# Optimization experiments

Measured on AMD Instinct MI355X. Metric: run time of the kernel, lower is better.

The kernel has to match this reference:

```python
import jax, jax.numpy as jnp
import numpy as np

DIM = 1024
HEADS = 8
DIM_HEAD = 64
INNER = HEADS * DIM_HEAD
SCALE = DIM_HEAD ** -0.5


def setup_inputs() -> dict:
    key = jax.random.key(0)
    ks = jax.random.split(key, 6)
    b, n = 2, 2048
    x = jax.random.normal(ks[0], (b, n, DIM), dtype=jnp.float32)
    rel_pos_bias = jax.random.normal(ks[1], (HEADS, n, n), dtype=jnp.float32)
    # learned params (Linear stores W as [out, in]; we keep [in, out] for x @ W)
    Wq = jax.random.normal(ks[2], (DIM, INNER), dtype=jnp.float32) * (DIM ** -0.5)
    Wkv = jax.random.normal(ks[3], (DIM, 2 * DIM_HEAD), dtype=jnp.float32) * (DIM ** -0.5)
    Wo = jax.random.normal(ks[4], (INNER, DIM), dtype=jnp.float32) * (INNER ** -0.5)
    bo = jax.random.normal(ks[5], (DIM,), dtype=jnp.float32) * 0.01
    return {"x": x, "rel_pos_bias": rel_pos_bias, "Wq": Wq, "Wkv": Wkv, "Wo": Wo, "bo": bo}


def reference(x, rel_pos_bias, Wq, Wkv, Wo, bo):
    b, n, _ = x.shape
    q = x @ Wq                       # [b, n, h*d]
    kv = x @ Wkv                     # [b, n, 2d] (multi-query: single shared kv head)
    k, v = kv[..., :DIM_HEAD], kv[..., DIM_HEAD:]
    q = q.reshape(b, n, HEADS, DIM_HEAD).transpose(0, 2, 1, 3) * SCALE  # [b, h, n, d]
    sim = jnp.einsum('bhid,bjd->bhij', q, k)
    sim = sim + rel_pos_bias         # bias broadcast over batch
    causal_mask = jnp.triu(jnp.ones((n, n), dtype=bool), k=1)
    neg = -jnp.finfo(sim.dtype).max
    sim = jnp.where(causal_mask, neg, sim)
    attn = jax.nn.softmax(sim, axis=-1)  # stable softmax (max-subtract internally)
    out = jnp.einsum('bhij,bjd->bhid', attn, v)
    out = out.transpose(0, 2, 1, 3).reshape(b, n, INNER)  # [b, n, h*d]
    return out @ Wo + bo
```

## Files before the change

kernel.cpp:

```cpp
#include <hip/hip_runtime.h>

#define NSEQ 2048
#define NB 2
#define NH 8
#define HD 64
#define DMODEL 1024
#define DINNER 512

#define SLOT_F 4224

typedef __attribute__((ext_vector_type(8))) short bf16x8;
typedef __attribute__((ext_vector_type(4))) float f32x4;

__device__ __forceinline__ ushort f2bf(float f) {
  uint u = __float_as_uint(f);
  uint r = (u + 0x7fffu + ((u >> 16) & 1u)) >> 16;
  return (ushort)r;
}

__device__ __forceinline__ void gld16(const ushort* g, ushort* l) {
  __builtin_amdgcn_global_load_lds(
      (const __attribute__((address_space(1))) uint*)g,
      (__attribute__((address_space(3))) uint*)l, 16, 0, 0);
}

__global__ __launch_bounds__(256) void transpose_cast_both_kernel(
    const float* __restrict__ Wq, const float* __restrict__ Wkv,
    const float* __restrict__ Wo, ushort* __restrict__ WT1sw,
    ushort* __restrict__ WoTsw) {
  __shared__ float t[64][65];
  const int id = blockIdx.x;
  const float *srcA, *srcB;
  int ldA, ldB, nsplit, k0, n0;
  ushort* tile;
  if (id < 160) {
    const int nt = id >> 4, kt = id & 15;
    k0 = kt * 64; n0 = nt * 64;
    srcA = Wq; srcB = Wkv; ldA = 512; ldB = 128; nsplit = 512;
    tile = WT1sw + (size_t)(nt * 16 + kt) * 4096;
  } else {
    const int u = id - 160;
    const int nt = u >> 3, kt = u & 7;
    k0 = kt * 64; n0 = nt * 64;
    srcA = Wo; srcB = Wo; ldA = 1024; ldB = 1024; nsplit = 1024;
    tile = WoTsw + (size_t)(nt * 8 + kt) * 4096;
  }
  const float* src; int ld, nb;
  if (n0 < nsplit) { src = srcA; ld = ldA; nb = n0; }
  else { src = srcB; ld = ldB; nb = n0 - nsplit; }
  const int r = threadIdx.x >> 4;
  const int c = (threadIdx.x & 15) * 4;
#pragma unroll
  for (int rr = r; rr < 64; rr += 16) {
    float4 v = *(const float4*)(src + (size_t)(k0 + rr) * ld + nb + c);
    t[rr][c + 0] = v.x; t[rr][c + 1] = v.y; t[rr][c + 2] = v.z; t[rr][c + 3] = v.w;
  }
  __syncthreads();
#pragma unroll
  for (int rr = r; rr < 64; rr += 16) {
    ushort4 o;
    o.x = f2bf(t[c + 0][rr]); o.y = f2bf(t[c + 1][rr]);
    o.z = f2bf(t[c + 2][rr]); o.w = f2bf(t[c + 3][rr]);
    *(ushort4*)(tile + (size_t)rr * 64 + (((c >> 3) ^ (rr & 7)) << 3) + (c & 7)) = o;
  }
}

__device__ __forceinline__ void stageA_f32(const float* __restrict__ src, int ld,
                                           int row0, int k0, ushort* lds, int tid) {
#pragma unroll
  for (int i = 0; i < 4; ++i) {
    const int cix = i * 256 + tid;
    const int row = cix >> 3, j = cix & 7;
    const float* p = src + (size_t)(row0 + row) * ld + k0 + j * 8;
    float4 a = *(const float4*)p;
    float4 b = *(const float4*)(p + 4);
    uint u0, u1, u2, u3;
    asm("v_cvt_pk_bf16_f32 %0, %1, %2" : "=v"(u0) : "v"(a.x), "v"(a.y));
    asm("v_cvt_pk_bf16_f32 %0, %1, %2" : "=v"(u1) : "v"(a.z), "v"(a.w));
    asm("v_cvt_pk_bf16_f32 %0, %1, %2" : "=v"(u2) : "v"(b.x), "v"(b.y));
    asm("v_cvt_pk_bf16_f32 %0, %1, %2" : "=v"(u3) : "v"(b.z), "v"(b.w));
    uint4 v; v.x = u0; v.y = u1; v.z = u2; v.w = u3;
    *(uint4*)((char*)lds + row * 128 + ((j ^ (row & 7)) << 4)) = v;
  }
}

__global__ __launch_bounds__(256) void qkv_mfma_kernel(
    const float* __restrict__ x, const ushort* __restrict__ WT1sw,
    ushort* __restrict__ qb, ushort* __restrict__ ksw, ushort* __restrict__ vsw) {
  __shared__ ushort As[128 * 64];
  __shared__ ushort Bs[64 * 64];
  const int tid = threadIdx.x;
  const int m0 = blockIdx.x * 128;
  const int nt = blockIdx.y;
  const int lane = tid & 63;
  const int w = tid >> 6;
  const int wr = w >> 1, wc = w & 1;
  const int lr = lane & 15, lg = lane >> 4;
  f32x4 acc[4][2];
#pragma unroll
  for (int a = 0; a < 4; ++a)
#pragma unroll
    for (int b = 0; b < 2; ++b) acc[a][b] = (f32x4){0.f, 0.f, 0.f, 0.f};
  for (int kt = 0; kt < 16; ++kt) {
    __syncthreads();
    {
      const ushort* bsrc =
          WT1sw + (size_t)(nt * 16 + kt) * 4096 + w * 1024 + lane * 8;
      gld16(bsrc, Bs + w * 1024);
      gld16(bsrc + 512, Bs + w * 1024 + 512);
    }
    stageA_f32(x, DMODEL, m0, kt * 64, As, tid);
    __syncthreads();
#pragma unroll
    for (int kk = 0; kk < 2; ++kk) {
      bf16x8 af[4], bfr[2];
#pragma unroll
      for (int mi = 0; mi < 4; ++mi) {
        const int r = wr * 64 + mi * 16 + lr;
        af[mi] = *(const bf16x8*)((char*)As + r * 128 + (((kk * 4 + lg) ^ (r & 7)) << 4));
      }
#pragma unroll
      for (int ni = 0; ni < 2; ++ni) {
        const int r = wc * 32 + ni * 16 + lr;
        bfr[ni] = *(const bf16x8*)((char*)Bs + r * 128 + (((kk * 4 + lg) ^ (r & 7)) << 4));
      }
#pragma unroll
      for (int mi = 0; mi < 4; ++mi)
#pragma unroll
        for (int ni = 0; ni < 2; ++ni)
          acc[mi][ni] = __builtin_amdgcn_mfma_f32_16x16x32_bf16(af[mi], bfr[ni],
                                                                acc[mi][ni], 0, 0, 0);
    }
  }
#pragma unroll
  for (int mi = 0; mi < 4; ++mi)
#pragma unroll
    for (int ni = 0; ni < 2; ++ni) {
      const int n = nt * 64 + wc * 32 + ni * 16 + lr;
#pragma unroll
      for (int r = 0; r < 4; ++r) {
        const int m = m0 + wr * 64 + mi * 16 + lg * 4 + r;
        const int bb = m >> 11, key = m & (NSEQ - 1);
        const float v = acc[mi][ni][r];
        if (nt < 8) {
          const int h = n >> 6, d = n & 63;
          qb[((size_t)((bb * NH + h) * NSEQ) + key) * HD + d] = f2bf(v * 0.125f);
        } else if (nt == 8) {
          const int d = n - DINNER;
          const int t = key >> 6, row = key & 63;
          ksw[(size_t)((bb * 32 + t) * 64 + row) * 64 +
              (((d >> 3) ^ (row & 7)) << 3) + (d & 7)] = f2bf(v);
        } else {
          const int d = n - DINNER - HD;
          const int pr = key >> 7, kk = key & 127;
          vsw[(size_t)((bb * 16 + pr) * 64 + d) * 128 +
              (((kk >> 3) ^ (d & 15)) << 3) + (kk & 7)] = f2bf(v);
        }
      }
    }
}

__global__ __launch_bounds__(256) void out_mfma_kernel(
    const ushort* __restrict__ obsw, const ushort* __restrict__ WoTsw,
    const float* __restrict__ bo, float* __restrict__ out) {
  __shared__ ushort As[2 * 128 * 64];
  __shared__ ushort Bs[2 * 64 * 64];
  const int tid = threadIdx.x;
  const int mt = blockIdx.x;
  const int nt = blockIdx.y;
  const int lane = tid & 63;
  const int w = tid >> 6;
  const int wr = w >> 1, wc = w & 1;
  const int lr = lane & 15, lg = lane >> 4;
  f32x4 acc[4][2];
#pragma unroll
  for (int a = 0; a < 4; ++a)
#pragma unroll
    for (int b = 0; b < 2; ++b) acc[a][b] = (f32x4){0.f, 0.f, 0.f, 0.f};

#define OISSUE(kt, buf)                                                       \
  {                                                                           \
    const ushort* _as =                                                       \
        obsw + (size_t)(mt * 8 + (kt)) * 8192 + w * 2048 + lane * 8;          \
    ushort* _ad = As + (buf) * 8192 + w * 2048;                               \
    gld16(_as, _ad);                                                          \
    gld16(_as + 512, _ad + 512);                                              \
    gld16(_as + 1024, _ad + 1024);                                            \
    gld16(_as + 1536, _ad + 1536);                                            \
    const ushort* _bs =                                                       \
        WoTsw + (size_t)(nt * 8 + (kt)) * 4096 + w * 1024 + lane * 8;         \
    ushort* _bd = Bs + (buf) * 4096 + w * 1024;                               \
    gld16(_bs, _bd);                                                          \
    gld16(_bs + 512, _bd + 512);                                              \
  }

  OISSUE(0, 0);
  OISSUE(1, 1);
  int cur = 0;
  for (int i = 0; i < 8; ++i) {
    if (i < 7) {
      asm volatile("s_waitcnt vmcnt(6)" ::: "memory");
    } else {
      asm volatile("s_waitcnt vmcnt(0)" ::: "memory");
    }
    __builtin_amdgcn_sched_barrier(0);
    __builtin_amdgcn_s_barrier();
    const char* Ac = (const char*)(As + cur * 8192);
    const char* Bc = (const char*)(Bs + cur * 4096);
    __builtin_amdgcn_s_setprio(1);
#pragma unroll
    for (int kk = 0; kk < 2; ++kk) {
      bf16x8 af[4], bfr[2];
#pragma unroll
      for (int mi = 0; mi < 4; ++mi) {
        const int r = wr * 64 + mi * 16 + lr;
        af[mi] = *(const bf16x8*)(Ac + r * 128 + (((kk * 4 + lg) ^ (r & 7)) << 4));
      }
#pragma unroll
      for (int ni = 0; ni < 2; ++ni) {
        const int r = wc * 32 + ni * 16 + lr;
        bfr[ni] = *(const bf16x8*)(Bc + r * 128 + (((kk * 4 + lg) ^ (r & 7)) << 4));
      }
#pragma unroll
      for (int mi = 0; mi < 4; ++mi)
#pragma unroll
        for (int ni = 0; ni < 2; ++ni)
          acc[mi][ni] = __builtin_amdgcn_mfma_f32_16x16x32_bf16(af[mi], bfr[ni],
                                                                acc[mi][ni], 0, 0, 0);
    }
    __builtin_amdgcn_s_setprio(0);
    __builtin_amdgcn_sched_barrier(0);
    __builtin_amdgcn_s_barrier();
    if (i + 2 < 8) OISSUE(i + 2, cur);
    cur ^= 1;
  }
#undef OISSUE
#pragma unroll
  for (int mi = 0; mi < 4; ++mi)
#pragma unroll
    for (int ni = 0; ni < 2; ++ni) {
      const int n = nt * 64 + wc * 32 + ni * 16 + lr;
      const float bias = bo[n];
#pragma unroll
      for (int r = 0; r < 4; ++r) {
        const int m = mt * 128 + wr * 64 + mi * 16 + lg * 4 + r;
        out[(size_t)m * DMODEL + n] = acc[mi][ni][r] + bias;
      }
    }
}

__global__ __launch_bounds__(256) void attn_mfma_kernel(
    const ushort* __restrict__ qb, const ushort* __restrict__ ksw,
    const ushort* __restrict__ vsw, const float* __restrict__ rpb,
    ushort* __restrict__ obsw, float* __restrict__ scratch) {
  __shared__ ushort Ks[2 * 128 * 64];
  __shared__ ushort Vs[2 * 64 * 128];
  __shared__ ushort Ps[4 * 16 * 128];
  const int tid = threadIdx.x;
  const int lane = tid & 63;
  const int w = tid >> 6;
  const int id = blockIdx.x;
  const int bh = id & 15;
  int qt, ch, p0, p1, partial;
  if (id < 256) {
    qt = 16 + (id >> 4); ch = 0; p0 = 0; p1 = 8; partial = 1;
  } else if (id < 512) {
    qt = 31 - ((id - 256) >> 4); ch = 1; p0 = 8; p1 = (qt >> 1) + 1; partial = 1;
  } else {
    qt = 15 - ((id - 512) >> 4); ch = 0; p0 = 0; p1 = (qt >> 1) + 1; partial = 0;
  }
  const int bb = bh >> 3, h = bh & 7;
  const int q0 = qt * 64;
  const int lr = lane & 15;
  const int lg = lane >> 4;
  const int pdiag = qt >> 1;

  const ushort* kpair = ksw + (size_t)bb * 32 * 64 * 64;
  const ushort* vpair = vsw + (size_t)bb * 16 * 64 * 128;
  const ushort* ksrcw = kpair + w * 2048 + lane * 8;
  const ushort* vsrcw = vpair + w * 2048 + lane * 8;
  ushort* kdstw = Ks + w * 2048;
  ushort* vdstw = Vs + w * 2048;

#define ISSUE(pp, bsel)                                                     \
  {                                                                         \
    const ushort* _ks = ksrcw + (size_t)(pp) * 8192;                        \
    const ushort* _vs = vsrcw + (size_t)(pp) * 8192;                        \
    ushort* _kd = kdstw + (bsel) * 8192;                                    \
    ushort* _vd = vdstw + (bsel) * 8192;                                    \
    gld16(_ks + 0 * 512, _kd + 0 * 512);                                    \
    gld16(_ks + 1 * 512, _kd + 1 * 512);                                    \
    gld16(_ks + 2 * 512, _kd + 2 * 512);                                    \
    gld16(_ks + 3 * 512, _kd + 3 * 512);                                    \
    gld16(_vs + 0 * 512, _vd + 0 * 512);                                    \
    gld16(_vs + 1 * 512, _vd + 1 * 512);                                    \
    gld16(_vs + 2 * 512, _vd + 2 * 512);                                    \
    gld16(_vs + 3 * 512, _vd + 3 * 512);                                    \
  }

#define LOAD_BIAS(pp, dst)                                                  \
  {                                                                         \
    const float* _br = rpb + (size_t)h * NSEQ * NSEQ +                      \
                       (size_t)(q0 + w * 16 + lg * 4) * NSEQ +              \
                       (pp) * 128 + lr;                                     \
    _Pragma("unroll")                                                       \
    for (int _ct = 0; _ct < 8; ++_ct)                                       \
      _Pragma("unroll")                                                     \
      for (int _r = 0; _r < 4; ++_r)                                        \
        dst[_ct][_r] = _br[(size_t)_r * NSEQ + _ct * 16];                   \
  }

  bf16x8 qf[2];
  {
    const ushort* qrow =
        qb + ((size_t)(bh * NSEQ) + q0 + w * 16 + lr) * HD + lg * 8;
    qf[0] = *(const bf16x8*)qrow;
    qf[1] = *(const bf16x8*)(qrow + 32);
  }
  f32x4 oacc[4];
  float m_run[4], l_run[4];
#pragma unroll
  for (int r = 0; r < 4; ++r) { m_run[r] = -1e30f; l_run[r] = 0.f; }
#pragma unroll
  for (int dt = 0; dt < 4; ++dt) oacc[dt] = (f32x4){0.f, 0.f, 0.f, 0.f};

  float bias_c[8][4], bias_n[8][4];

  ISSUE(p0, 0);
  LOAD_BIAS(p0, bias_c);
  ISSUE(p0 + 1, 1);
  int curb = 0;

  for (int p = p0; p < p1; ++p) {
    if (p < p1 - 1) {
      asm volatile("s_waitcnt vmcnt(40)" ::: "memory");
    } else {
      asm volatile("s_waitcnt vmcnt(32)" ::: "memory");
    }
    __builtin_amdgcn_sched_barrier(0);
    __builtin_amdgcn_s_barrier();

    const char* Kc = (const char*)(Ks + curb * 8192);
    const char* Vc = (const char*)(Vs + curb * 8192);
    f32x4 s[8];
    __builtin_amdgcn_s_setprio(1);
#pragma unroll
    for (int ct = 0; ct < 8; ++ct) {
      s[ct] = (f32x4){0.f, 0.f, 0.f, 0.f};
      const int krow = ct * 16 + lr;
#pragma unroll
      for (int kk = 0; kk < 2; ++kk) {
        bf16x8 kf = *(const bf16x8*)(Kc + krow * 128 +
                                     (((kk * 4 + lg) ^ (krow & 7)) << 4));
        s[ct] = __builtin_amdgcn_mfma_f32_16x16x32_bf16(qf[kk], kf, s[ct], 0, 0, 0);
      }
    }
    __builtin_amdgcn_s_setprio(0);
    if (p + 1 < p1) LOAD_BIAS(p + 1, bias_n);
#pragma unroll
    for (int ct = 0; ct < 8; ++ct)
#pragma unroll
      for (int r = 0; r < 4; ++r) s[ct][r] += bias_c[ct][r];
    if (p == pdiag) {
      const int qrel = q0 + w * 16 + lg * 4;
#pragma unroll
      for (int ct = 0; ct < 8; ++ct) {
        const int kg = p * 128 + ct * 16 + lr;
#pragma unroll
        for (int r = 0; r < 4; ++r)
          if (kg > qrel + r) s[ct][r] = -1e30f;
      }
    }
    float fac[4];
#pragma unroll
    for (int r = 0; r < 4; ++r) {
      float mt = s[0][r];
#pragma unroll
      for (int ct = 1; ct < 8; ++ct) mt = fmaxf(mt, s[ct][r]);
#pragma unroll
      for (int msk = 1; msk < 16; msk <<= 1)
        mt = fmaxf(mt, __shfl_xor(mt, msk, 64));
      const float m_new = fmaxf(m_run[r], mt);
      fac[r] = __expf(m_run[r] - m_new);
      m_run[r] = m_new;
      float ls = 0.f;
#pragma unroll
      for (int ct = 0; ct < 8; ++ct) {
        const float pv = __expf(s[ct][r] - m_new);
        s[ct][r] = pv;
        ls += pv;
      }
#pragma unroll
      for (int msk = 1; msk < 16; msk <<= 1) ls += __shfl_xor(ls, msk, 64);
      l_run[r] = l_run[r] * fac[r] + ls;
    }
#pragma unroll
    for (int dt = 0; dt < 4; ++dt)
#pragma unroll
      for (int r = 0; r < 4; ++r) oacc[dt][r] *= fac[r];
    char* Pw = (char*)Ps + w * 4096;
#pragma unroll
    for (int ct = 0; ct < 8; ++ct) {
      uint u01, u23;
      asm("v_cvt_pk_bf16_f32 %0, %1, %2" : "=v"(u01) : "v"(s[ct][0]), "v"(s[ct][1]));
      asm("v_cvt_pk_bf16_f32 %0, %1, %2" : "=v"(u23) : "v"(s[ct][2]), "v"(s[ct][3]));
      const int cbyte = (ct * 16 + lr) * 2;
      const int chv = cbyte >> 4, off = cbyte & 15;
      const int r0 = lg * 4;
      *(ushort*)(Pw + (r0 + 0) * 256 + (((chv ^ (r0 + 0)) << 4) | off)) = (ushort)u01;
      *(ushort*)(Pw + (r0 + 1) * 256 + (((chv ^ (r0 + 1)) << 4) | off)) = (ushort)(u01 >> 16);
      *(ushort*)(Pw + (r0 + 2) * 256 + (((chv ^ (r0 + 2)) << 4) | off)) = (ushort)u23;
      *(ushort*)(Pw + (r0 + 3) * 256 + (((chv ^ (r0 + 3)) << 4) | off)) = (ushort)(u23 >> 16);
    }
    __builtin_amdgcn_s_setprio(1);
#pragma unroll
    for (int kk = 0; kk < 4; ++kk) {
      bf16x8 pf = *(const bf16x8*)(Pw + lr * 256 + (((kk * 4 + lg) ^ lr) << 4));
#pragma unroll
      for (int dt = 0; dt < 4; ++dt) {
        const int vrow = dt * 16 + lr;
        bf16x8 vf = *(const bf16x8*)(Vc + vrow * 256 +
                                     (((kk * 4 + lg) ^ (vrow & 15)) << 4));
        oacc[dt] =
            __builtin_amdgcn_mfma_f32_16x16x32_bf16(pf, vf, oacc[dt], 0, 0, 0);
      }
    }
    __builtin_amdgcn_s_setprio(0);
    __builtin_amdgcn_sched_barrier(0);
    __builtin_amdgcn_s_barrier();
    if (p + 2 < p1) ISSUE(p + 2, curb);
    if (p + 1 < p1) {
#pragma unroll
      for (int ct = 0; ct < 8; ++ct)
#pragma unroll
        for (int r = 0; r < 4; ++r) bias_c[ct][r] = bias_n[ct][r];
    }
    curb ^= 1;
  }
#undef ISSUE
#undef LOAD_BIAS
  if (!partial) {
#pragma unroll
    for (int r = 0; r < 4; ++r) {
      const int qg = q0 + w * 16 + lg * 4 + r;
      const int m = bb * NSEQ + qg;
      const int row = m & 127, mt = m >> 7;
      const int rs = row & 7;
      ushort* tb = obsw + (size_t)(mt * 8 + h) * 8192 + row * 64;
      const float inv = 1.0f / l_run[r];
#pragma unroll
      for (int dt = 0; dt < 4; ++dt) {
        const int d = dt * 16 + lr;
        tb[(((d >> 3) ^ rs) << 3) + (d & 7)] = f2bf(oacc[dt][r] * inv);
      }
    }
  } else {
    float* slot =
        scratch + (size_t)((bh * 16 + (qt - 16)) * 2 + ch) * SLOT_F;
#pragma unroll
    for (int r = 0; r < 4; ++r) {
      const int row = w * 16 + lg * 4 + r;
#pragma unroll
      for (int dt = 0; dt < 4; ++dt)
        slot[row * 64 + dt * 16 + lr] = oacc[dt][r];
      if (lr == 0) {
        slot[4096 + row] = m_run[r];
        slot[4160 + row] = l_run[r];
      }
    }
  }
}

__global__ __launch_bounds__(256) void attn_merge_kernel(
    const float* __restrict__ scratch, ushort* __restrict__ obsw) {
  const int bid = blockIdx.x;
  const int bh = bid >> 4;
  const int qt = 16 + (bid & 15);
  const int bb = bh >> 3, h = bh & 7;
  const float* s0 = scratch + (size_t)((bh * 16 + (qt - 16)) * 2) * SLOT_F;
  const float* s1 = s0 + SLOT_F;
  const int t = threadIdx.x;
  const int r = t >> 2;
  const int c0 = (t & 3) * 16;
  const float m0 = s0[4096 + r], m1 = s1[4096 + r];
  const float M = fmaxf(m0, m1);
  const float sc0 = __expf(m0 - M), sc1 = __expf(m1 - M);
  const float L = s0[4160 + r] * sc0 + s1[4160 + r] * sc1;
  const float inv = 1.0f / L;
  ushort tmp[16];
#pragma unroll
  for (int j4 = 0; j4 < 4; ++j4) {
    float4 a = *(const float4*)(s0 + r * 64 + c0 + j4 * 4);
    float4 b = *(const float4*)(s1 + r * 64 + c0 + j4 * 4);
    tmp[j4 * 4 + 0] = f2bf((a.x * sc0 + b.x * sc1) * inv);
    tmp[j4 * 4 + 1] = f2bf((a.y * sc0 + b.y * sc1) * inv);
    tmp[j4 * 4 + 2] = f2bf((a.z * sc0 + b.z * sc1) * inv);
    tmp[j4 * 4 + 3] = f2bf((a.w * sc0 + b.w * sc1) * inv);
  }
  const int m = bb * NSEQ + qt * 64 + r;
  const int row = m & 127, mt = m >> 7;
  const int rs = row & 7;
  ushort* tb = obsw + (size_t)(mt * 8 + h) * 8192 + row * 64;
  *(uint4*)(tb + ((((c0 >> 3) + 0) ^ rs) << 3)) = *(const uint4*)&tmp[0];
  *(uint4*)(tb + ((((c0 >> 3) + 1) ^ rs) << 3)) = *(const uint4*)&tmp[8];
}

extern "C" void kernel_launch(void* const* d_in, const int* in_sizes, int n_in,
                              void* d_out, int out_size, void* d_ws, size_t ws_size,
                              hipStream_t stream) {
  (void)in_sizes; (void)n_in; (void)out_size; (void)ws_size;
  const float* x = (const float*)d_in[0];
  const float* rpb = (const float*)d_in[1];
  const float* Wq = (const float*)d_in[2];
  const float* Wkv = (const float*)d_in[3];
  const float* Wo = (const float*)d_in[4];
  const float* bo = (const float*)d_in[5];
  float* out = (float*)d_out;

  ushort* qbb = (ushort*)d_ws;
  ushort* ksw = qbb + (size_t)NB * NH * NSEQ * HD;
  ushort* vsw = ksw + (size_t)NB * NSEQ * HD;
  ushort* obsw = vsw + (size_t)NB * NSEQ * HD;
  ushort* WT1sw = obsw + (size_t)NB * NSEQ * DINNER;
  ushort* WoTsw = WT1sw + (size_t)640 * DMODEL;
  float* scratch = (float*)(WoTsw + (size_t)DMODEL * DINNER);

  transpose_cast_both_kernel<<<dim3(288), 256, 0, stream>>>(Wq, Wkv, Wo, WT1sw,
                                                            WoTsw);
  qkv_mfma_kernel<<<dim3(32, 10), 256, 0, stream>>>(x, WT1sw, qbb, ksw, vsw);
  attn_mfma_kernel<<<dim3(768), 256, 0, stream>>>(qbb, ksw, vsw, rpb, obsw,
                                                  scratch);
  attn_merge_kernel<<<dim3(256), 256, 0, stream>>>(scratch, obsw);
  out_mfma_kernel<<<dim3(32, 16), 256, 0, stream>>>(obsw, WoTsw, bo, out);
}
```

Measured before the change: 83.04 us.

## Pre-cast x to swizzled bf16 and widen QKV/out GEMM tiles to 128x128

x is now converted to bf16 once, in swizzled tiles inside the prep kernel, so the QKV GEMM no longer re-reads and converts fp32 x for every N tile. The QKV GEMM now uses double-buffered async global-to-LDS loads with a software pipeline like the out GEMM. Both GEMMs move from 128x64 to 128x128 block tiles, halving their grid sizes and raising reuse of each loaded tile. In exchange there is an extra bf16 round trip of x through memory, more accumulator registers, more LDS per block, and fewer blocks, which can lower occupancy.

```diff
diff --git a/kernel.cpp b/kernel.cpp
--- a/kernel.cpp
+++ b/kernel.cpp
@@ -24,22 +24,45 @@
       (__attribute__((address_space(3))) uint*)l, 16, 0, 0);
 }
 
-__global__ __launch_bounds__(256) void transpose_cast_both_kernel(
-    const float* __restrict__ Wq, const float* __restrict__ Wkv,
-    const float* __restrict__ Wo, ushort* __restrict__ WT1sw,
+__global__ __launch_bounds__(256) void prep_kernel(
+    const float* __restrict__ x, const float* __restrict__ Wq,
+    const float* __restrict__ Wkv, const float* __restrict__ Wo,
+    ushort* __restrict__ xsw, ushort* __restrict__ WT1sw,
     ushort* __restrict__ WoTsw) {
   __shared__ float t[64][65];
   const int id = blockIdx.x;
+  const int tid = threadIdx.x;
+  if (id < 512) {
+    const int mt = id >> 4, kt = id & 15;
+    ushort* tile = xsw + (size_t)(mt * 16 + kt) * 8192;
+#pragma unroll
+    for (int i = 0; i < 4; ++i) {
+      const int cix = i * 256 + tid;
+      const int row = cix >> 3, j = cix & 7;
+      const float* p = x + (size_t)(mt * 128 + row) * DMODEL + kt * 64 + j * 8;
+      float4 a = *(const float4*)p;
+      float4 b = *(const float4*)(p + 4);
+      uint u0, u1, u2, u3;
+      asm("v_cvt_pk_bf16_f32 %0, %1, %2" : "=v"(u0) : "v"(a.x), "v"(a.y));
+      asm("v_cvt_pk_bf16_f32 %0, %1, %2" : "=v"(u1) : "v"(a.z), "v"(a.w));
+      asm("v_cvt_pk_bf16_f32 %0, %1, %2" : "=v"(u2) : "v"(b.x), "v"(b.y));
+      asm("v_cvt_pk_bf16_f32 %0, %1, %2" : "=v"(u3) : "v"(b.z), "v"(b.w));
+      uint4 v; v.x = u0; v.y = u1; v.z = u2; v.w = u3;
+      *(uint4*)(tile + (size_t)row * 64 + ((j ^ (row & 7)) << 3)) = v;
+    }
+    return;
+  }
   const float *srcA, *srcB;
   int ldA, ldB, nsplit, k0, n0;
   ushort* tile;
-  if (id < 160) {
-    const int nt = id >> 4, kt = id & 15;
+  if (id < 672) {
+    const int u = id - 512;
+    const int nt = u >> 4, kt = u & 15;
     k0 = kt * 64; n0 = nt * 64;
     srcA = Wq; srcB = Wkv; ldA = 512; ldB = 128; nsplit = 512;
     tile = WT1sw + (size_t)(nt * 16 + kt) * 4096;
   } else {
-    const int u = id - 160;
+    const int u = id - 672;
     const int nt = u >> 3, kt = u & 7;
     k0 = kt * 64; n0 = nt * 64;
     srcA = Wo; srcB = Wo; ldA = 1024; ldB = 1024; nsplit = 1024;
@@ -48,8 +71,8 @@
   const float* src; int ld, nb;
   if (n0 < nsplit) { src = srcA; ld = ldA; nb = n0; }
   else { src = srcB; ld = ldB; nb = n0 - nsplit; }
-  const int r = threadIdx.x >> 4;
-  const int c = (threadIdx.x & 15) * 4;
+  const int r = tid >> 4;
+  const int c = (tid & 15) * 4;
 #pragma unroll
   for (int rr = r; rr < 64; rr += 16) {
     float4 v = *(const float4*)(src + (size_t)(k0 + rr) * ld + nb + c);
@@ -65,87 +88,98 @@
   }
 }
 
-__device__ __forceinline__ void stageA_f32(const float* __restrict__ src, int ld,
-                                           int row0, int k0, ushort* lds, int tid) {
-#pragma unroll
-  for (int i = 0; i < 4; ++i) {
-    const int cix = i * 256 + tid;
-    const int row = cix >> 3, j = cix & 7;
-    const float* p = src + (size_t)(row0 + row) * ld + k0 + j * 8;
-    float4 a = *(const float4*)p;
-    float4 b = *(const float4*)(p + 4);
-    uint u0, u1, u2, u3;
-    asm("v_cvt_pk_bf16_f32 %0, %1, %2" : "=v"(u0) : "v"(a.x), "v"(a.y));
-    asm("v_cvt_pk_bf16_f32 %0, %1, %2" : "=v"(u1) : "v"(a.z), "v"(a.w));
-    asm("v_cvt_pk_bf16_f32 %0, %1, %2" : "=v"(u2) : "v"(b.x), "v"(b.y));
-    asm("v_cvt_pk_bf16_f32 %0, %1, %2" : "=v"(u3) : "v"(b.z), "v"(b.w));
-    uint4 v; v.x = u0; v.y = u1; v.z = u2; v.w = u3;
-    *(uint4*)((char*)lds + row * 128 + ((j ^ (row & 7)) << 4)) = v;
-  }
-}
-
 __global__ __launch_bounds__(256) void qkv_mfma_kernel(
-    const float* __restrict__ x, const ushort* __restrict__ WT1sw,
+    const ushort* __restrict__ xsw, const ushort* __restrict__ WT1sw,
     ushort* __restrict__ qb, ushort* __restrict__ ksw, ushort* __restrict__ vsw) {
-  __shared__ ushort As[128 * 64];
-  __shared__ ushort Bs[64 * 64];
+  __shared__ ushort As[2 * 128 * 64];
+  __shared__ ushort Bs[2 * 128 * 64];
   const int tid = threadIdx.x;
-  const int m0 = blockIdx.x * 128;
+  const int mt = blockIdx.x;
   const int nt = blockIdx.y;
   const int lane = tid & 63;
   const int w = tid >> 6;
   const int wr = w >> 1, wc = w & 1;
   const int lr = lane & 15, lg = lane >> 4;
-  f32x4 acc[4][2];
+  f32x4 acc[4][4];
 #pragma unroll
   for (int a = 0; a < 4; ++a)
 #pragma unroll
-    for (int b = 0; b < 2; ++b) acc[a][b] = (f32x4){0.f, 0.f, 0.f, 0.f};
-  for (int kt = 0; kt < 16; ++kt) {
-    __syncthreads();
-    {
-      const ushort* bsrc =
-          WT1sw + (size_t)(nt * 16 + kt) * 4096 + w * 1024 + lane * 8;
-      gld16(bsrc, Bs + w * 1024);
-      gld16(bsrc + 512, Bs + w * 1024 + 512);
-    }
-    stageA_f32(x, DMODEL, m0, kt * 64, As, tid);
-    __syncthreads();
+    for (int b = 0; b < 4; ++b) acc[a][b] = (f32x4){0.f, 0.f, 0.f, 0.f};
+
+#define QISSUE(kt, buf)                                                       \
+  {                                                                           \
+    const ushort* _as =                                                       \
+        xsw + (size_t)(mt * 16 + (kt)) * 8192 + w * 2048 + lane * 8;          \
+    ushort* _ad = As + (buf) * 8192 + w * 2048;                               \
+    gld16(_as, _ad);                                                          \
+    gld16(_as + 512, _ad + 512);                                              \
+    gld16(_as + 1024, _ad + 1024);                                            \
+    gld16(_as + 1536, _ad + 1536);                                            \
+    const ushort* _bs = WT1sw +                                               \
+        (size_t)((nt * 2 + (w >> 1)) * 16 + (kt)) * 4096 + (w & 1) * 2048 +   \
+        lane * 8;                                                             \
+    ushort* _bd = Bs + (buf) * 8192 + w * 2048;                               \
+    gld16(_bs, _bd);                                                          \
+    gld16(_bs + 512, _bd + 512);                                              \
+    gld16(_bs + 1024, _bd + 1024);                                            \
+    gld16(_bs + 1536, _bd + 1536);                                            \
+  }
+
+  QISSUE(0, 0);
+  QISSUE(1, 1);
+  int cur = 0;
+  for (int i = 0; i < 16; ++i) {
+    if (i < 15) {
+      asm volatile("s_waitcnt vmcnt(8)" ::: "memory");
+    } else {
+      asm volatile("s_waitcnt vmcnt(0)" ::: "memory");
+    }
+    __builtin_amdgcn_sched_barrier(0);
+    __builtin_amdgcn_s_barrier();
+    const char* Ac = (const char*)(As + cur * 8192);
+    const char* Bc = (const char*)(Bs + cur * 8192);
+    __builtin_amdgcn_s_setprio(1);
 #pragma unroll
     for (int kk = 0; kk < 2; ++kk) {
-      bf16x8 af[4], bfr[2];
+      bf16x8 af[4], bfr[4];
 #pragma unroll
       for (int mi = 0; mi < 4; ++mi) {
         const int r = wr * 64 + mi * 16 + lr;
-        af[mi] = *(const bf16x8*)((char*)As + r * 128 + (((kk * 4 + lg) ^ (r & 7)) << 4));
-      }
-#pragma unroll
-      for (int ni = 0; ni < 2; ++ni) {
-        const int r = wc * 32 + ni * 16 + lr;
-        bfr[ni] = *(const bf16x8*)((char*)Bs + r * 128 + (((kk * 4 + lg) ^ (r & 7)) << 4));
+        af[mi] = *(const bf16x8*)(Ac + r * 128 + (((kk * 4 + lg) ^ (r & 7)) << 4));
+      }
+#pragma unroll
+      for (int ni = 0; ni < 4; ++ni) {
+        const int r = wc * 64 + ni * 16 + lr;
+        bfr[ni] = *(const bf16x8*)(Bc + r * 128 + (((kk * 4 + lg) ^ (r & 7)) << 4));
       }
 #pragma unroll
       for (int mi = 0; mi < 4; ++mi)
 #pragma unroll
-        for (int ni = 0; ni < 2; ++ni)
+        for (int ni = 0; ni < 4; ++ni)
           acc[mi][ni] = __builtin_amdgcn_mfma_f32_16x16x32_bf16(af[mi], bfr[ni],
                                                                 acc[mi][ni], 0, 0, 0);
     }
-  }
+    __builtin_amdgcn_s_setprio(0);
+    __builtin_amdgcn_sched_barrier(0);
+    __builtin_amdgcn_s_barrier();
+    if (i + 2 < 16) QISSUE(i + 2, cur);
+    cur ^= 1;
+  }
+#undef QISSUE
 #pragma unroll
   for (int mi = 0; mi < 4; ++mi)
 #pragma unroll
-    for (int ni = 0; ni < 2; ++ni) {
-      const int n = nt * 64 + wc * 32 + ni * 16 + lr;
+    for (int ni = 0; ni < 4; ++ni) {
+      const int n = nt * 128 + wc * 64 + ni * 16 + lr;
 #pragma unroll
       for (int r = 0; r < 4; ++r) {
-        const int m = m0 + wr * 64 + mi * 16 + lg * 4 + r;
+        const int m = mt * 128 + wr * 64 + mi * 16 + lg * 4 + r;
         const int bb = m >> 11, key = m & (NSEQ - 1);
         const float v = acc[mi][ni][r];
-        if (nt < 8) {
+        if (n < DINNER) {
           const int h = n >> 6, d = n & 63;
           qb[((size_t)((bb * NH + h) * NSEQ) + key) * HD + d] = f2bf(v * 0.125f);
-        } else if (nt == 8) {
+        } else if (n < DINNER + HD) {
           const int d = n - DINNER;
           const int t = key >> 6, row = key & 63;
           ksw[(size_t)((bb * 32 + t) * 64 + row) * 64 +
@@ -164,7 +198,7 @@
     const ushort* __restrict__ obsw, const ushort* __restrict__ WoTsw,
     const float* __restrict__ bo, float* __restrict__ out) {
   __shared__ ushort As[2 * 128 * 64];
-  __shared__ ushort Bs[2 * 64 * 64];
+  __shared__ ushort Bs[2 * 128 * 64];
   const int tid = threadIdx.x;
   const int mt = blockIdx.x;
   const int nt = blockIdx.y;
@@ -172,11 +206,11 @@
   const int w = tid >> 6;
   const int wr = w >> 1, wc = w & 1;
   const int lr = lane & 15, lg = lane >> 4;
-  f32x4 acc[4][2];
+  f32x4 acc[4][4];
 #pragma unroll
   for (int a = 0; a < 4; ++a)
 #pragma unroll
-    for (int b = 0; b < 2; ++b) acc[a][b] = (f32x4){0.f, 0.f, 0.f, 0.f};
+    for (int b = 0; b < 4; ++b) acc[a][b] = (f32x4){0.f, 0.f, 0.f, 0.f};
 
 #define OISSUE(kt, buf)                                                       \
   {                                                                           \
@@ -187,11 +221,14 @@
     gld16(_as + 512, _ad + 512);                                              \
     gld16(_as + 1024, _ad + 1024);                                            \
     gld16(_as + 1536, _ad + 1536);                                            \
-    const ushort* _bs =                                                       \
-        WoTsw + (size_t)(nt * 8 + (kt)) * 4096 + w * 1024 + lane * 8;         \
-    ushort* _bd = Bs + (buf) * 4096 + w * 1024;                               \
+    const ushort* _bs = WoTsw +                                               \
+        (size_t)((nt * 2 + (w >> 1)) * 8 + (kt)) * 4096 + (w & 1) * 2048 +    \
+        lane * 8;                                                             \
+    ushort* _bd = Bs + (buf) * 8192 + w * 2048;                               \
     gld16(_bs, _bd);                                                          \
     gld16(_bs + 512, _bd + 512);                                              \
+    gld16(_bs + 1024, _bd + 1024);                                            \
+    gld16(_bs + 1536, _bd + 1536);                                            \
   }
 
   OISSUE(0, 0);
@@ -199,32 +236,32 @@
   int cur = 0;
   for (int i = 0; i < 8; ++i) {
     if (i < 7) {
-      asm volatile("s_waitcnt vmcnt(6)" ::: "memory");
+      asm volatile("s_waitcnt vmcnt(8)" ::: "memory");
     } else {
       asm volatile("s_waitcnt vmcnt(0)" ::: "memory");
     }
     __builtin_amdgcn_sched_barrier(0);
     __builtin_amdgcn_s_barrier();
     const char* Ac = (const char*)(As + cur * 8192);
-    const char* Bc = (const char*)(Bs + cur * 4096);
+    const char* Bc = (const char*)(Bs + cur * 8192);
     __builtin_amdgcn_s_setprio(1);
 #pragma unroll
     for (int kk = 0; kk < 2; ++kk) {
-      bf16x8 af[4], bfr[2];
+      bf16x8 af[4], bfr[4];
 #pragma unroll
       for (int mi = 0; mi < 4; ++mi) {
         const int r = wr * 64 + mi * 16 + lr;
         af[mi] = *(const bf16x8*)(Ac + r * 128 + (((kk * 4 + lg) ^ (r & 7)) << 4));
       }
 #pragma unroll
-      for (int ni = 0; ni < 2; ++ni) {
-        const int r = wc * 32 + ni * 16 + lr;
+      for (int ni = 0; ni < 4; ++ni) {
+        const int r = wc * 64 + ni * 16 + lr;
         bfr[ni] = *(const bf16x8*)(Bc + r * 128 + (((kk * 4 + lg) ^ (r & 7)) << 4));
       }
 #pragma unroll
       for (int mi = 0; mi < 4; ++mi)
 #pragma unroll
-        for (int ni = 0; ni < 2; ++ni)
+        for (int ni = 0; ni < 4; ++ni)
           acc[mi][ni] = __builtin_amdgcn_mfma_f32_16x16x32_bf16(af[mi], bfr[ni],
                                                                 acc[mi][ni], 0, 0, 0);
     }
@@ -238,8 +275,8 @@
 #pragma unroll
   for (int mi = 0; mi < 4; ++mi)
 #pragma unroll
-    for (int ni = 0; ni < 2; ++ni) {
-      const int n = nt * 64 + wc * 32 + ni * 16 + lr;
+    for (int ni = 0; ni < 4; ++ni) {
+      const int n = nt * 128 + wc * 64 + ni * 16 + lr;
       const float bias = bo[n];
 #pragma unroll
       for (int r = 0; r < 4; ++r) {
@@ -521,15 +558,15 @@
   ushort* ksw = qbb + (size_t)NB * NH * NSEQ * HD;
   ushort* vsw = ksw + (size_t)NB * NSEQ * HD;
   ushort* obsw = vsw + (size_t)NB * NSEQ * HD;
-  ushort* WT1sw = obsw + (size_t)NB * NSEQ * DINNER;
+  ushort* xsw = obsw + (size_t)NB * NSEQ * DINNER;
+  ushort* WT1sw = xsw + (size_t)NB * NSEQ * DMODEL;
   ushort* WoTsw = WT1sw + (size_t)640 * DMODEL;
   float* scratch = (float*)(WoTsw + (size_t)DMODEL * DINNER);
 
-  transpose_cast_both_kernel<<<dim3(288), 256, 0, stream>>>(Wq, Wkv, Wo, WT1sw,
-                                                            WoTsw);
-  qkv_mfma_kernel<<<dim3(32, 10), 256, 0, stream>>>(x, WT1sw, qbb, ksw, vsw);
+  prep_kernel<<<dim3(800), 256, 0, stream>>>(x, Wq, Wkv, Wo, xsw, WT1sw, WoTsw);
+  qkv_mfma_kernel<<<dim3(32, 5), 256, 0, stream>>>(xsw, WT1sw, qbb, ksw, vsw);
   attn_mfma_kernel<<<dim3(768), 256, 0, stream>>>(qbb, ksw, vsw, rpb, obsw,
                                                   scratch);
   attn_merge_kernel<<<dim3(256), 256, 0, stream>>>(scratch, obsw);
-  out_mfma_kernel<<<dim3(32, 16), 256, 0, stream>>>(obsw, WoTsw, bo, out);
-}
+  out_mfma_kernel<<<dim3(32, 8), 256, 0, stream>>>(obsw, WoTsw, bo, out);
+}
```

Measured after the change: 86.62 us. 1.04x slower.
